# Performance work log

Hardware: AMD Instinct MI355X
Metric: run time of the kernel (lower is better)

The kernel has to match this reference:

```python
import jax, jax.numpy as jnp
from jax import lax
import numpy as np

B, H, W = 8, 512, 512
HW = H * W  # sentinel label for non-mask pixels


def _label_components(mask):
    """4-connectivity connected-component labeling (min flat-index per component).
    mask: [H,W] bool. Returns [HW] int32 labels; non-mask pixels get label HW.
    Label propagation + pointer jumping -> O(log diameter) iterations."""
    idx = jnp.arange(HW, dtype=jnp.int32).reshape(H, W)
    lab0 = jnp.where(mask, idx, HW)

    def step(lab):
        p = jnp.pad(lab, 1, mode='constant', constant_values=HW)
        nb = jnp.minimum(jnp.minimum(p[:-2, 1:-1], p[2:, 1:-1]),
                         jnp.minimum(p[1:-1, :-2], p[1:-1, 2:]))
        new = jnp.where(mask, jnp.minimum(lab, nb), HW)
        flat = new.reshape(-1)
        flat_ext = jnp.concatenate([flat, jnp.array([HW], dtype=flat.dtype)])
        new = jnp.minimum(flat, flat_ext[flat]).reshape(H, W)  # pointer jump
        return jnp.where(mask, new, HW)

    def cond(state):
        return state[1]

    def body(state):
        lab, _ = state
        new = step(lab)
        return new, jnp.any(new != lab)

    lab, _ = lax.while_loop(cond, body, (lab0, jnp.array(True)))
    return lab.reshape(-1)


def _keep_large(mask):
    """Keep pixels belonging to components with area > max_area/2 (matches
    ndi.label + ndi.sum + thresholded relabel; ndi.sum scaling by 255/1 cancels)."""
    labels = _label_components(mask)  # [HW]
    counts = jax.ops.segment_sum(mask.reshape(-1).astype(jnp.float32), labels,
                                 num_segments=HW + 1)  # counts[HW]=0 (non-mask contributes 0)
    max_area = counts.max()
    keep = mask.reshape(-1) & (counts[labels] > 0.5 * max_area)
    return keep.reshape(mask.shape)


def _masked_ce(logits, target):
    """CrossEntropyLoss(ignore_index=255, reduction='mean'). logits [B,C,H,W], target [B,H,W]."""
    logp = jax.nn.log_softmax(logits, axis=1)
    valid = target != 255
    tc = jnp.where(valid, target, 0)
    nll = -jnp.take_along_axis(logp, tc[:, None], axis=1)[:, 0]  # [B,H,W]
    denom = jnp.maximum(jnp.sum(valid), 1).astype(logp.dtype)
    return jnp.sum(jnp.where(valid, nll, 0.0)) / denom


def setup_inputs() -> dict:
    key = jax.random.key(0)
    k1, k2 = jax.random.split(key)
    preds = jax.random.normal(k1, (3, B, 2, H, W), dtype=jnp.float32)
    cams = jax.random.uniform(k2, (B, 1, H, W), dtype=jnp.float32)
    return {"preds": preds, "cams": cams}


def reference(preds, cams):
    cam = cams[:, 0]                      # [B,H,W]
    bg_mask = cam >= 0.2                  # pixels left at 255 in bg_label (the labeled regions)
    fg_mask = cam > 0.6                   # pixels set to 1 in fg_label
    keep_bg = jax.vmap(_keep_large)(bg_mask)
    keep_fg = jax.vmap(_keep_large)(fg_mask)
    bg_t = jnp.where(keep_bg, 255, 0).astype(jnp.int32)   # large uncertain regions ignored
    fg_t = jnp.where(keep_fg, 1, 255).astype(jnp.int32)   # small/non-fg ignored
    loss = jnp.float32(0.0)
    for i in range(preds.shape[0]):       # weight (1**i / 1) == 1
        loss = loss + _masked_ce(preds[i], fg_t) + _masked_ce(preds[i], bg_t)
    return loss
```

## Files before the change

kernel.cpp:

```cpp
#include <hip/hip_runtime.h>
#include <hip/hip_bf16.h>
#include <math.h>

#define Bsz    8
#define Wdim   512
#define HWv    (512 * 512)
#define LOG2HW 18
#define NIMG   16
#define TILE   64
#define TPIX   (TILE * TILE)
#define RCAP   2048


__device__ __forceinline__ int uf_find(int* L, int x) {
  int p = L[x];
  while (p != x) {
    int gp = L[p];
    if (gp != p) atomicMin(&L[x], gp);
    x = gp;
    p = L[x];
  }
  return x;
}

__device__ __forceinline__ int find_ro(const int* __restrict__ L, int x) {
  int p = L[x];
  while (p != x) { x = p; p = L[x]; }
  return x;
}

__device__ __forceinline__ void uf_union(int* L, int a, int b) {
  a = uf_find(L, a);
  b = uf_find(L, b);
  while (a != b) {
    if (a < b) { int t = a; a = b; b = t; }
    int old = atomicMin(&L[a], b);
    if (old == a) return;
    a = old;
  }
}


__global__ __launch_bounds__(1024) void k_local(const float* __restrict__ cams,
    int* __restrict__ parent, int* __restrict__ areas,
    unsigned short* __restrict__ L16, unsigned int* __restrict__ rootPack,
    int* __restrict__ rootCnt, int* __restrict__ bL, int* __restrict__ bR,
    int* __restrict__ bT, int* __restrict__ bB) {
  int b    = blockIdx.x >> 6;
  int tile = blockIdx.x & 63;
  int oy = (tile >> 3) * TILE, ox = (tile & 7) * TILE;
  int tid = threadIdx.x, lane = tid & 63;

  __shared__ int P[2][TPIX];
  __shared__ int A[2][TPIX];
  __shared__ int rc[2];
  if (tid < 2) rc[tid] = 0;

  #pragma unroll
  for (int it = 0; it < 4; ++it) {
    int i  = it * 1024 + tid;
    int ly = i >> 6;
    float c = cams[(b << LOG2HW) + ((oy + ly) << 9) + ox + lane];
    #pragma unroll
    for (int m = 0; m < 2; ++m) {
      bool msk = m ? (c > 0.6f) : (c >= 0.2f);
      unsigned long long bm = __ballot(msk);
      int par = -1;
      if (msk) {
        unsigned long long below = (1ULL << lane) - 1ULL;
        unsigned long long z = (~bm) & below;
        int rs = z ? (64 - __clzll(z)) : 0;
        par = (ly << 6) + rs;
      }
      P[m][i] = par;
      A[m][i] = 0;
    }
  }
  __syncthreads();

  #pragma unroll
  for (int it = 0; it < 4; ++it) {
    int i = it * 1024 + tid;
    if (i >= TILE) {
      #pragma unroll
      for (int m = 0; m < 2; ++m) {
        if (P[m][i] >= 0 && P[m][i - TILE] >= 0) {
          bool skip = (lane > 0) && (P[m][i - 1] >= 0) && (P[m][i - TILE - 1] >= 0);
          if (!skip) uf_union(P[m], i, i - TILE);
        }
      }
    }
  }
  __syncthreads();

  #pragma unroll
  for (int it = 0; it < 4; ++it) {
    int i = it * 1024 + tid;
    #pragma unroll
    for (int m = 0; m < 2; ++m) {
      bool msk = P[m][i] >= 0;
      unsigned long long bm = __ballot(msk);
      int rs = 0;
      if (msk) {
        unsigned long long below = (1ULL << lane) - 1ULL;
        unsigned long long z = (~bm) & below;
        rs = z ? (64 - __clzll(z)) : 0;
      }
      bool isStart = msk && (rs == lane);
      int r = -1;
      if (isStart) r = find_ro(P[m], i);
      int root = __shfl(r, rs);
      if (msk) P[m][i] = root;
      if (isStart) {
        unsigned long long t = (~bm) >> lane;
        int runlen = t ? (__ffsll((long long)t) - 1) : (64 - lane);
        atomicAdd(&A[m][root], runlen);
      }
    }
  }
  __syncthreads();

  #pragma unroll
  for (int it = 0; it < 4; ++it) {
    int i  = it * 1024 + tid;
    int ly = i >> 6, lx = i & 63;
    int g  = ((oy + ly) << 9) + ox + lx;
    #pragma unroll
    for (int m = 0; m < 2; ++m) {
      int imgm = m * 8 + b;
      int p = P[m][i];
      L16[((size_t)imgm << LOG2HW) + g] = (p < 0) ? (unsigned short)0xFFFF
                                                  : (unsigned short)p;
      if (p == i) {
        int slot = atomicAdd(&rc[m], 1);
        parent[(imgm << LOG2HW) + g] = g;
        areas [(imgm << LOG2HW) + g] = 0;
        rootPack[(((imgm << 6) + tile) * RCAP) + slot] =
            ((unsigned)i << 13) | (unsigned)A[m][i];
      }
    }
  }
  __syncthreads();
  if (tid < 2) rootCnt[(((tid * 8 + b) << 6) + tile)] = rc[tid];
  if (tid < 512) {
    int m = tid >> 8, rem = tid & 255, e = rem >> 6, k = rem & 63;
    int i = (e == 0) ? (k << 6) : (e == 1) ? ((k << 6) + 63)
          : (e == 2) ? k : ((63 << 6) + k);
    int p = P[m][i];
    int val = (p < 0) ? -1 : (((oy + (p >> 6)) << 9) + ox + (p & 63));
    int idx = (((m * 8 + b) << 6) + tile) * 64 + k;
    if (e == 0) bL[idx] = val; else if (e == 1) bR[idx] = val;
    else if (e == 2) bT[idx] = val; else bB[idx] = val;
  }
}

__global__ void k_border(int* __restrict__ parent, const int* __restrict__ bL,
                         const int* __restrict__ bR, const int* __restrict__ bT,
                         const int* __restrict__ bB, int* __restrict__ maxa,
                         double* __restrict__ sums, int* __restrict__ counts) {
  if (blockIdx.x == 0) {
    if (threadIdx.x < NIMG) maxa[threadIdx.x] = 0;
    if (threadIdx.x < 2) { sums[threadIdx.x] = 0.0; counts[threadIdx.x] = 0; }
  }
  int t = blockIdx.x * blockDim.x + threadIdx.x;
  int img = t / 7168;
  int r   = t - img * 7168;
  int* Lp = parent + (img << LOG2HW);
  if (r < 3584) {
    int v = r >> 6, y = r & 63;
    int tXl = v >> 3, tYv = v & 7;
    int tileL = tYv * 8 + tXl;
    int baseR = ((img << 6) + tileL) * 64;
    int baseL = ((img << 6) + tileL + 1) * 64;
    int pr = bR[baseR + y], qr = bL[baseL + y];
    if (pr >= 0 && qr >= 0) {
      bool skip = (y > 0) && (bR[baseR + y - 1] >= 0) && (bL[baseL + y - 1] >= 0);
      if (!skip) uf_union(Lp, pr, qr);
    }
  } else {
    int r2 = r - 3584;
    int h = r2 >> 6, x = r2 & 63;
    int tYt = h >> 3, tX = h & 7;
    int tileT = tYt * 8 + tX;
    int baseB = ((img << 6) + tileT) * 64;
    int baseT = ((img << 6) + tileT + 8) * 64;
    int pr = bB[baseB + x], qr = bT[baseT + x];
    if (pr >= 0 && qr >= 0) {
      bool skip = (x > 0) && (bB[baseB + x - 1] >= 0) && (bT[baseT + x - 1] >= 0);
      if (!skip) uf_union(Lp, pr, qr);
    }
  }
}

__global__ void k_flatten(int* __restrict__ parent, int* __restrict__ areas,
                          const unsigned int* __restrict__ rootPack,
                          int* __restrict__ rootF, const int* __restrict__ rootCnt) {
  int lt = blockIdx.x;
  int imgm = lt >> 6, tile = lt & 63;
  int oy = (tile >> 3) * TILE, ox = (tile & 7) * TILE;
  int cnt = rootCnt[lt];
  const int* Lp = parent + (imgm << LOG2HW);
  for (int k = threadIdx.x; k < cnt; k += blockDim.x) {
    unsigned pk = rootPack[lt * RCAP + k];
    int loc = pk >> 13, area = pk & 8191;
    int gr = ((oy + (loc >> 6)) << 9) + ox + (loc & 63);
    int f = find_ro(Lp, gr);
    atomicAdd(&areas[(imgm << LOG2HW) + f], area);
    rootF[lt * RCAP + k] = f;
  }
}

__global__ void k_max(const int* __restrict__ areas, int* __restrict__ rootF,
                      const int* __restrict__ rootCnt, int* __restrict__ maxa) {
  int lt = blockIdx.x;
  int imgm = lt >> 6;
  int cnt = rootCnt[lt];
  int m = 0;
  for (int k = threadIdx.x; k < cnt; k += blockDim.x) {
    int tot = areas[(imgm << LOG2HW) + rootF[lt * RCAP + k]];
    rootF[lt * RCAP + k] = tot;
    m = max(m, tot);
  }
  #pragma unroll
  for (int off = 32; off > 0; off >>= 1)
    m = max(m, __shfl_down(m, off));
  __shared__ int lm[4];
  int wave = threadIdx.x >> 6;
  if ((threadIdx.x & 63) == 0) lm[wave] = m;
  __syncthreads();
  if (threadIdx.x == 0) {
    int bm = max(max(lm[0], lm[1]), max(lm[2], lm[3]));
    if (bm > 0) atomicMax(&maxa[imgm], bm);
  }
}

__global__ __launch_bounds__(1024) void k_keepce(const float* __restrict__ preds,
    const unsigned short* __restrict__ L16, const unsigned int* __restrict__ rootPack,
    const int* __restrict__ rootF, const int* __restrict__ rootCnt,
    const int* __restrict__ maxa, double* __restrict__ sums, int* __restrict__ counts) {
  int b = blockIdx.x >> 6, tile = blockIdx.x & 63;
  int oy = (tile >> 3) * TILE, ox = (tile & 7) * TILE;
  __shared__ unsigned short V[2][TPIX];
  int mx0 = maxa[b], mx1 = maxa[8 + b];
  #pragma unroll
  for (int m = 0; m < 2; ++m) {
    int lt = (((m * 8 + b) << 6) + tile);
    int cnt = rootCnt[lt];
    int mxm = m ? mx1 : mx0;
    for (int k = threadIdx.x; k < cnt; k += 1024) {
      unsigned pk = rootPack[lt * RCAP + k];
      int tot = rootF[lt * RCAP + k];
      V[m][pk >> 13] = (2 * tot > mxm) ? 1 : 0;
    }
  }
  __syncthreads();

  int i0 = threadIdx.x << 2;
  int ly = i0 >> 6, lx = i0 & 63;
  int g  = ((oy + ly) << 9) + ox + lx;
  ushort4 ub4 = *(const ushort4*)&L16[((size_t)b << LOG2HW) + g];
  ushort4 uf4 = *(const ushort4*)&L16[((size_t)(8 + b) << LOG2HW) + g];
  float4 A0[3], A1[3];
  #pragma unroll
  for (int p = 0; p < 3; p++) {
    const float* pb = preds + ((size_t)((p * Bsz + b) * 2) << LOG2HW);
    A0[p] = *(const float4*)&pb[g];
    A1[p] = *(const float4*)&pb[HWv + g];
  }
  unsigned short lb[4] = {ub4.x, ub4.y, ub4.z, ub4.w};
  unsigned short lf[4] = {uf4.x, uf4.y, uf4.z, uf4.w};
  bool vf[4], vb[4];
  #pragma unroll
  for (int j = 0; j < 4; j++) {
    bool kb = (lb[j] != 0xFFFF) && (V[0][lb[j] & 4095] != 0);
    bool kf = (lf[j] != 0xFFFF) && (V[1][lf[j] & 4095] != 0);
    vb[j] = !kb;
    vf[j] = kf;
  }
  int cf = (int)vf[0] + vf[1] + vf[2] + vf[3];
  int cb = (int)vb[0] + vb[1] + vb[2] + vb[3];
  float sfg = 0.f, sbg = 0.f;
  #pragma unroll
  for (int p = 0; p < 3; p++) {
    float d[4] = {A0[p].x - A1[p].x, A0[p].y - A1[p].y,
                  A0[p].z - A1[p].z, A0[p].w - A1[p].w};
    #pragma unroll
    for (int j = 0; j < 4; j++) {
      float sp = logf(1.f + expf(-fabsf(d[j])));
      sfg += vf[j] ? (fmaxf(d[j], 0.f) + sp) : 0.f;
      sbg += vb[j] ? (fmaxf(-d[j], 0.f) + sp) : 0.f;
    }
  }
  #pragma unroll
  for (int off = 32; off > 0; off >>= 1) {
    sfg += __shfl_down(sfg, off);
    sbg += __shfl_down(sbg, off);
    cf  += __shfl_down(cf, off);
    cb  += __shfl_down(cb, off);
  }
  __shared__ float lsf[16], lsb[16];
  __shared__ int   lcf[16], lcb[16];
  int wave = threadIdx.x >> 6;
  if ((threadIdx.x & 63) == 0) {
    lsf[wave] = sfg; lsb[wave] = sbg; lcf[wave] = cf; lcb[wave] = cb;
  }
  __syncthreads();
  if (threadIdx.x == 0) {
    float tf = 0.f, tb = 0.f; int af_ = 0, ab_ = 0;
    #pragma unroll
    for (int w = 0; w < 16; w++) { tf += lsf[w]; tb += lsb[w]; af_ += lcf[w]; ab_ += lcb[w]; }
    atomicAdd(&sums[0], (double)tf);
    atomicAdd(&sums[1], (double)tb);
    atomicAdd(&counts[0], af_);
    atomicAdd(&counts[1], ab_);
  }
}

__global__ void k_final(const double* __restrict__ sums, const int* __restrict__ counts,
                        float* __restrict__ out) {
  if (threadIdx.x == 0 && blockIdx.x == 0) {
    double df = counts[0] > 0 ? (double)counts[0] : 1.0;
    double db = counts[1] > 0 ? (double)counts[1] : 1.0;
    out[0] = (float)(sums[0] / df + sums[1] / db);
  }
}

extern "C" void kernel_launch(void* const* d_in, const int* in_sizes, int n_in,
                              void* d_out, int out_size, void* d_ws, size_t ws_size,
                              hipStream_t stream) {
  (void)in_sizes; (void)n_in; (void)out_size; (void)ws_size;
  const float* preds = (const float*)d_in[0];
  const float* cams  = (const float*)d_in[1];
  float* out = (float*)d_out;

  int* parent = (int*)d_ws;
  int* areas  = parent + (NIMG << LOG2HW);
  unsigned short* L16 = (unsigned short*)(areas + (NIMG << LOG2HW));
  unsigned int* rootPack = (unsigned int*)(L16 + ((size_t)NIMG << LOG2HW));
  int* rootF   = (int*)(rootPack + NIMG * 64 * RCAP);
  int* rootCnt = rootF + NIMG * 64 * RCAP;
  int* bL = rootCnt + NIMG * 64;
  int* bR = bL + NIMG * 64 * 64;
  int* bT = bR + NIMG * 64 * 64;
  int* bB = bT + NIMG * 64 * 64;
  int* maxa = bB + NIMG * 64 * 64;
  double* sums = (double*)(maxa + 16);
  int* counts  = (int*)(sums + 2);

  k_local  <<<Bsz * 64, 1024, 0, stream>>>(cams, parent, areas, L16, rootPack,
                                           rootCnt, bL, bR, bT, bB);
  k_border <<<NIMG * 7168 / 256, 256, 0, stream>>>(parent, bL, bR, bT, bB,
                                                   maxa, sums, counts);
  k_flatten<<<NIMG * 64, 256, 0, stream>>>(parent, areas, rootPack, rootF, rootCnt);
  k_max    <<<NIMG * 64, 256, 0, stream>>>(areas, rootF, rootCnt, maxa);
  k_keepce <<<Bsz * 64, 1024, 0, stream>>>(preds, L16, rootPack, rootF, rootCnt,
                                           maxa, sums, counts);
  k_final  <<<1, 64, 0, stream>>>(sums, counts, out);
}
```

Measured before the change: 168.5 us.

## Fuse flatten with max via atomic return value and finalize with ticket

Merges the flatten and max kernels by tracking each component's running maximum from the value returned by the area atomicAdd. This is valid because the final atomic on each root yields the full total. The keep kernel now reads component totals directly from the areas array. The final scalar reduction moves into the last-finishing block of the keep/CE kernel through an atomic ticket counter. Together these remove two kernel launches and their inter-kernel gaps, at the cost of an extra global gather of areas and threadfence-based completion ordering.

```diff
diff --git a/kernel.cpp b/kernel.cpp
--- a/kernel.cpp
+++ b/kernel.cpp
@@ -3,7 +3,6 @@
 #include <math.h>
 
 #define Bsz    8
-#define Wdim   512
 #define HWv    (512 * 512)
 #define LOG2HW 18
 #define NIMG   16
@@ -112,8 +111,8 @@
       int root = __shfl(r, rs);
       if (msk) P[m][i] = root;
       if (isStart) {
-        unsigned long long t = (~bm) >> lane;
-        int runlen = t ? (__ffsll((long long)t) - 1) : (64 - lane);
+        unsigned long long t2 = (~bm) >> lane;
+        int runlen = t2 ? (__ffsll((long long)t2) - 1) : (64 - lane);
         atomicAdd(&A[m][root], runlen);
       }
     }
@@ -157,10 +156,12 @@
 __global__ void k_border(int* __restrict__ parent, const int* __restrict__ bL,
                          const int* __restrict__ bR, const int* __restrict__ bT,
                          const int* __restrict__ bB, int* __restrict__ maxa,
-                         double* __restrict__ sums, int* __restrict__ counts) {
+                         double* __restrict__ sums, int* __restrict__ counts,
+                         int* __restrict__ ticket) {
   if (blockIdx.x == 0) {
     if (threadIdx.x < NIMG) maxa[threadIdx.x] = 0;
     if (threadIdx.x < 2) { sums[threadIdx.x] = 0.0; counts[threadIdx.x] = 0; }
+    if (threadIdx.x == 2) *ticket = 0;
   }
   int t = blockIdx.x * blockDim.x + threadIdx.x;
   int img = t / 7168;
@@ -192,34 +193,24 @@
   }
 }
 
-__global__ void k_flatten(int* __restrict__ parent, int* __restrict__ areas,
+__global__ void k_flatmax(int* __restrict__ parent, int* __restrict__ areas,
                           const unsigned int* __restrict__ rootPack,
-                          int* __restrict__ rootF, const int* __restrict__ rootCnt) {
+                          int* __restrict__ rootF, const int* __restrict__ rootCnt,
+                          int* __restrict__ maxa) {
   int lt = blockIdx.x;
   int imgm = lt >> 6, tile = lt & 63;
   int oy = (tile >> 3) * TILE, ox = (tile & 7) * TILE;
   int cnt = rootCnt[lt];
   const int* Lp = parent + (imgm << LOG2HW);
+  int m = 0;
   for (int k = threadIdx.x; k < cnt; k += blockDim.x) {
     unsigned pk = rootPack[lt * RCAP + k];
-    int loc = pk >> 13, area = pk & 8191;
+    int loc = pk >> 13, area = (int)(pk & 8191u);
     int gr = ((oy + (loc >> 6)) << 9) + ox + (loc & 63);
     int f = find_ro(Lp, gr);
-    atomicAdd(&areas[(imgm << LOG2HW) + f], area);
+    int old = atomicAdd(&areas[(imgm << LOG2HW) + f], area);
+    m = max(m, old + area);
     rootF[lt * RCAP + k] = f;
-  }
-}
-
-__global__ void k_max(const int* __restrict__ areas, int* __restrict__ rootF,
-                      const int* __restrict__ rootCnt, int* __restrict__ maxa) {
-  int lt = blockIdx.x;
-  int imgm = lt >> 6;
-  int cnt = rootCnt[lt];
-  int m = 0;
-  for (int k = threadIdx.x; k < cnt; k += blockDim.x) {
-    int tot = areas[(imgm << LOG2HW) + rootF[lt * RCAP + k]];
-    rootF[lt * RCAP + k] = tot;
-    m = max(m, tot);
   }
   #pragma unroll
   for (int off = 32; off > 0; off >>= 1)
@@ -237,19 +228,23 @@
 __global__ __launch_bounds__(1024) void k_keepce(const float* __restrict__ preds,
     const unsigned short* __restrict__ L16, const unsigned int* __restrict__ rootPack,
     const int* __restrict__ rootF, const int* __restrict__ rootCnt,
-    const int* __restrict__ maxa, double* __restrict__ sums, int* __restrict__ counts) {
+    const int* __restrict__ areas, const int* __restrict__ maxa,
+    double* __restrict__ sums, int* __restrict__ counts,
+    int* __restrict__ ticket, float* __restrict__ out) {
   int b = blockIdx.x >> 6, tile = blockIdx.x & 63;
   int oy = (tile >> 3) * TILE, ox = (tile & 7) * TILE;
   __shared__ unsigned short V[2][TPIX];
   int mx0 = maxa[b], mx1 = maxa[8 + b];
   #pragma unroll
   for (int m = 0; m < 2; ++m) {
-    int lt = (((m * 8 + b) << 6) + tile);
+    int imgm = m * 8 + b;
+    int lt = (imgm << 6) + tile;
     int cnt = rootCnt[lt];
     int mxm = m ? mx1 : mx0;
     for (int k = threadIdx.x; k < cnt; k += 1024) {
       unsigned pk = rootPack[lt * RCAP + k];
-      int tot = rootF[lt * RCAP + k];
+      int f = rootF[lt * RCAP + k];
+      int tot = areas[(imgm << LOG2HW) + f];
       V[m][pk >> 13] = (2 * tot > mxm) ? 1 : 0;
     }
   }
@@ -313,15 +308,14 @@
     atomicAdd(&sums[1], (double)tb);
     atomicAdd(&counts[0], af_);
     atomicAdd(&counts[1], ab_);
-  }
-}
-
-__global__ void k_final(const double* __restrict__ sums, const int* __restrict__ counts,
-                        float* __restrict__ out) {
-  if (threadIdx.x == 0 && blockIdx.x == 0) {
-    double df = counts[0] > 0 ? (double)counts[0] : 1.0;
-    double db = counts[1] > 0 ? (double)counts[1] : 1.0;
-    out[0] = (float)(sums[0] / df + sums[1] / db);
+    __threadfence();
+    int done = atomicAdd(ticket, 1);
+    if (done == (int)gridDim.x - 1) {
+      __threadfence();
+      double df = counts[0] > 0 ? (double)counts[0] : 1.0;
+      double db = counts[1] > 0 ? (double)counts[1] : 1.0;
+      out[0] = (float)(sums[0] / df + sums[1] / db);
+    }
   }
 }
 
@@ -346,14 +340,14 @@
   int* maxa = bB + NIMG * 64 * 64;
   double* sums = (double*)(maxa + 16);
   int* counts  = (int*)(sums + 2);
+  int* ticket  = counts + 2;
 
   k_local  <<<Bsz * 64, 1024, 0, stream>>>(cams, parent, areas, L16, rootPack,
                                            rootCnt, bL, bR, bT, bB);
   k_border <<<NIMG * 7168 / 256, 256, 0, stream>>>(parent, bL, bR, bT, bB,
-                                                   maxa, sums, counts);
-  k_flatten<<<NIMG * 64, 256, 0, stream>>>(parent, areas, rootPack, rootF, rootCnt);
-  k_max    <<<NIMG * 64, 256, 0, stream>>>(areas, rootF, rootCnt, maxa);
+                                                   maxa, sums, counts, ticket);
+  k_flatmax<<<NIMG * 64, 256, 0, stream>>>(parent, areas, rootPack, rootF,
+                                           rootCnt, maxa);
   k_keepce <<<Bsz * 64, 1024, 0, stream>>>(preds, L16, rootPack, rootF, rootCnt,
-                                           maxa, sums, counts);
-  k_final  <<<1, 64, 0, stream>>>(sums, counts, out);
-}
+                                           areas, maxa, sums, counts, ticket, out);
+}
```

Result: no change. 170.8 us (+1.4%).
